# Kernel tuning notes

Measured on AMD Instinct MI355X. Metric: run time of the kernel, lower is better.

The kernel has to match this reference:

```python
import jax, jax.numpy as jnp
import numpy as np

B, L, H, HEADS, N_NODE = 1024, 200, 128, 8, 200000
MAXN = L + 1  # max_n_node
D = H // HEADS
EPS = 1e-12


def setup_inputs() -> dict:
    key = jax.random.key(0)
    ks = jax.random.split(key, 20)
    lengths = jax.random.randint(ks[0], (B,), 1, L + 1)
    mask = (jnp.arange(L)[None, :] < lengths[:, None]).astype(jnp.int32)  # contiguous 1s
    alias_inputs = jax.random.randint(ks[1], (B, L), 0, MAXN)
    items = jax.random.randint(ks[2], (B, MAXN), 0, N_NODE)

    def lin_w(k, o, i):
        return (jax.random.normal(k, (o, i), jnp.float32) * 0.1)

    inp = dict(
        alias_inputs=alias_inputs,
        items=items,
        mask=mask,
        emb_W=jax.random.normal(ks[3], (N_NODE, H), jnp.float32) * 0.1,
        # LastAttenion params
        W0=lin_w(ks[4], H, H), b0=jax.random.normal(ks[5], (H,), jnp.float32) * 0.1,
        W1=lin_w(ks[6], H, H), b1=jax.random.normal(ks[7], (H,), jnp.float32) * 0.1,
        W2=lin_w(ks[8], H, H), b2=jax.random.normal(ks[9], (H,), jnp.float32) * 0.1,
        # linear_q[0] (last_k = 1)
        Wq=lin_w(ks[10], H, H), bq=jax.random.normal(ks[11], (H,), jnp.float32) * 0.1,
        # linear_transform (2H -> H)
        Wt=lin_w(ks[12], H, 2 * H), bt=jax.random.normal(ks[13], (H,), jnp.float32) * 0.1,
        ln_g=jax.random.normal(ks[14], (H,), jnp.float32) * 0.1,
        ln_b=jax.random.normal(ks[15], (H,), jnp.float32) * 0.1,
    )
    return inp


def reference(alias_inputs, items, mask, emb_W, W0, b0, W1, b1, W2, b2, Wq, bq, Wt, bt, ln_g, ln_b):
    maskf = mask.astype(jnp.float32)
    # hidden = normalize(embedding(items)); dropout off (eval)
    hidden = emb_W[items]                                                  # [B, MAXN, H]
    hidden = hidden / (jnp.linalg.norm(hidden, axis=-1, keepdims=True) + EPS)
    # per-batch gather: seq_hidden[b, t] = hidden[b, alias_inputs[b, t]]
    seq = jnp.take_along_axis(hidden, alias_inputs[..., None], axis=1)     # [B, L, H]
    seq = seq * maskf[..., None]
    seq = seq / (jnp.linalg.norm(seq, axis=-1, keepdims=True) + EPS)
    # compute_scores
    lengths = mask.sum(1)
    last_idx = lengths - 1                                                 # >= 0 (lengths >= 1)
    ht_last = seq[jnp.arange(B), last_idx]                                 # [B, H]  (ht0 too)
    hts = (ht_last @ Wq.T + bq)[:, None, :]                                # [B, 1, H]
    # torch.norm over dim=1 (size 1) == elementwise abs
    hts = hts / (jnp.linalg.norm(hts, axis=1, keepdims=True) + EPS)
    # LastAttenion (last_k = 1, no lp-pool, eval dropout off)
    q0 = (hts @ W0.T + b0).reshape(B * HEADS, 1, D)                        # [B*h, 1, d]
    q1 = (seq @ W1.T + b1).reshape(B * HEADS, L, D)                        # [B*h, L, d]
    q2 = (seq @ W2.T + b2).reshape(B, L, HEADS, D)                         # [B, L, h, d]
    alpha = jax.nn.sigmoid(jnp.einsum('bkd,bld->bkl', q0, q1))             # [B*h, 1, L]
    alpha = alpha.reshape(B, HEADS, L).transpose(0, 2, 1)                  # [B, L, h]
    alpha = jax.nn.softmax(2.0 * alpha, axis=1)
    a = jnp.sum((alpha[..., None] * q2).reshape(B, L, H) * maskf[..., None], axis=1)  # [B, H]
    # layernorm eps=1e-8
    mu = a.mean(-1, keepdims=True)
    var = ((a - mu) ** 2).mean(-1, keepdims=True)
    a = (a - mu) / jnp.sqrt(var + 1e-8) * ln_g + ln_b
    a = jnp.concatenate([a, ht_last], axis=1) @ Wt.T + bt                  # [B, H]
    # norm=True branch
    a = a / (jnp.linalg.norm(a, axis=1, keepdims=True) + EPS)
    b = emb_W[1:]
    b = b / (jnp.linalg.norm(b, axis=1, keepdims=True) + EPS)
    return a, b.T                                                          # [B,H], [H, N_NODE-1]
```

## Files before the change

### kernel.cpp

```cpp
#include <hip/hip_runtime.h>
#include <math.h>

typedef unsigned int uint;
typedef unsigned short ushort;

__device__ __forceinline__ float b2f(ushort u){
  union { uint i; float f; } v; v.i = ((uint)u) << 16; return v.f;
}
__device__ __forceinline__ ushort f2b(float f){
  union { float f; uint i; } v; v.f = f;
  uint i = v.i;
  i += 0x7fffu + ((i >> 16) & 1u);
  return (ushort)(i >> 16);
}
__device__ __forceinline__ float wred(float v){
  #pragma unroll
  for (int s = 32; s > 0; s >>= 1) v += __shfl_xor(v, s, 64);
  return v;
}
__device__ __forceinline__ float gred16(float v){
  v += __shfl_xor(v, 1, 64);
  v += __shfl_xor(v, 2, 64);
  v += __shfl_xor(v, 4, 64);
  v += __shfl_xor(v, 8, 64);
  return v;
}
__device__ __forceinline__ float sane(float v){ return isfinite(v) ? v : 0.f; }
__device__ __forceinline__ int iclamp(int v, int lo, int hi){ return v < lo ? lo : (v > hi ? hi : v); }
__device__ __forceinline__ void cp8(float d[8], const float s[8]){
  #pragma unroll
  for (int e = 0; e < 8; ++e) d[e] = s[e];
}

__device__ __forceinline__ void load_raw8(const void* emb, int isf, int it, int p, float x[8]){
  if (it >= 0){
    if (isf){
      const float4* q = (const float4*)((const float*)emb + (size_t)it * 128);
      float4 u = q[p * 2], u2 = q[p * 2 + 1];
      x[0] = u.x; x[1] = u.y; x[2] = u.z; x[3] = u.w;
      x[4] = u2.x; x[5] = u2.y; x[6] = u2.z; x[7] = u2.w;
    } else {
      uint4 u = ((const uint4*)((const ushort*)emb + (size_t)it * 128))[p];
      x[0] = b2f((ushort)u.x); x[1] = b2f((ushort)(u.x >> 16));
      x[2] = b2f((ushort)u.y); x[3] = b2f((ushort)(u.y >> 16));
      x[4] = b2f((ushort)u.z); x[5] = b2f((ushort)(u.z >> 16));
      x[6] = b2f((ushort)u.w); x[7] = b2f((ushort)(u.w >> 16));
    }
  } else {
    #pragma unroll
    for (int e = 0; e < 8; ++e) x[e] = 0.f;
  }
}

__device__ __forceinline__ int detect_isf(const void* emb, int t, int* s_flag){
  if (t == 0) *s_flag = 0;
  __syncthreads();
  if (t < 64){
    uint4 u = ((const uint4*)emb)[t];
    uint w[4] = { u.x, u.y, u.z, u.w };
    int bad = 0;
    #pragma unroll
    for (int e = 0; e < 4; ++e){
      float v0 = fabsf(b2f((ushort)w[e]));
      float v1 = fabsf(b2f((ushort)(w[e] >> 16)));
      if (!(v0 <= 1e4f) || !(v1 <= 1e4f)) bad = 1;
    }
    if (bad) *s_flag = 1;
  }
  __syncthreads();
  return *s_flag;
}

#define OUTB 131072

#define C_W0T 0
#define C_W1  16384
#define C_W2T 32768
#define C_WQT 49152
#define C_WTT 65536
#define C_B0  98304
#define C_B1  98432
#define C_B2  98560
#define C_BQ  98688
#define C_BT  98816
#define C_G   98944
#define C_BB  99072
#define C_TOT 99200

#define KFUSED_SMEM 22784

#define NB_MAIN 1024
#define NB_BOUT 3125
#define NB_TOT  4149

__global__ __launch_bounds__(256) void k_wts(
    const void* __restrict__ emb,
    const void* W0, const void* b0, const void* W1, const void* b1,
    const void* W2, const void* b2, const void* Wq, const void* bq,
    const void* Wt, const void* bt, const void* g, const void* bb,
    float* __restrict__ wts){
  __shared__ int s_flag;
  const int t = threadIdx.x;
  const int isf = detect_isf(emb, t, &s_flag);
  int j = blockIdx.x * 256 + t;
  if (j >= C_TOT) return;
  const void* src; int si;
  if (j < 16384)      { int k = j >> 7, h = j & 127; src = W0; si = h * 128 + k; }
  else if (j < 32768) { src = W1; si = j - 16384; }
  else if (j < 49152) { int i = j - 32768; int k = i >> 7, h = i & 127; src = W2; si = h * 128 + k; }
  else if (j < 65536) { int i = j - 49152; int k = i >> 7, h = i & 127; src = Wq; si = h * 128 + k; }
  else if (j < 98304) { int i = j - 65536; int k = i >> 7, h = i & 127; src = Wt; si = h * 256 + k; }
  else {
    int i = j - 98304; int arr = i >> 7;
    const void* tab[7] = { b0, b1, b2, bq, bt, g, bb };
    src = tab[arr]; si = i & 127;
  }
  wts[j] = isf ? ((const float*)src)[si] : b2f(((const ushort*)src)[si]);
}

__device__ void bout_block(const void* __restrict__ emb, int isf,
                           void* __restrict__ outv, int bb, int t, char* dsm){
  float* tile = (float*)dsm;
  const int gid = t >> 4, p = t & 15;
  const int base = bb * 64;
  for (int pass = 0; pass < 2; ++pass){
    const int pb = base + pass * 32;
    if (pass) __syncthreads();
    for (int i = gid; i < 32; i += 16){
      int gi = pb + i;
      if (gi < 199999){
        float x[8];
        load_raw8(emb, isf, gi + 1, p, x);
        float ss = 0.f;
        #pragma unroll
        for (int e = 0; e < 8; ++e) ss += x[e] * x[e];
        ss = gred16(ss);
        float inv = 1.f / (sqrtf(ss) + 1e-12f);
        #pragma unroll
        for (int e = 0; e < 8; ++e) tile[i * 129 + p * 8 + e] = x[e] * inv;
      }
    }
    __syncthreads();
    #pragma unroll
    for (int it = 0; it < 16; ++it){
      int idx = it * 256 + t;
      int h = idx >> 5, n = idx & 31;
      int gi = pb + n;
      if (gi < 199999){
        float val = sane(tile[n * 129 + h]);
        if (isf){
          float* op = (float*)outv + OUTB + (size_t)h * 199999 + gi;
          __builtin_nontemporal_store(val, op);
        } else {
          ushort* op = (ushort*)outv + OUTB + (size_t)h * 199999 + gi;
          __builtin_nontemporal_store(f2b(val), op);
        }
      }
    }
  }
}

__global__ __launch_bounds__(256) void k_fused(
    const int* __restrict__ alias_, const int* __restrict__ items,
    const int* __restrict__ mask, const void* __restrict__ emb,
    const float* __restrict__ wts, void* __restrict__ outv){
  extern __shared__ __align__(16) char dsm[];
  __shared__ int s_flag;
  __shared__ float s_X0[128], s_ht[128], s_a[128], s_hts[128];
  __shared__ float s_c1[64];
  __shared__ float s_T[8], s_Tp[64];
  __shared__ float s_red[16];
  __shared__ float s_nrm[200];
  __shared__ int   s_it[200];
  __shared__ int   s_item;

  const int t = threadIdx.x;
  const int isf = detect_isf(emb, t, &s_flag);

  const int bid = blockIdx.x;
  const int m = (bid * NB_MAIN) / NB_TOT;
  const bool is_main = ((bid + 1) * NB_MAIN) / NB_TOT > m;
  if (!is_main){
    bout_block(emb, isf, outv, bid - m, t, dsm);
    return;
  }
  const int b = m;

  ushort* s_w1p   = (ushort*)dsm;
  float*  s_part  = (float*)dsm;
  float*  s_alpha = (float*)(dsm + 16384);

  const int wv = t >> 6, gid = t >> 4, p = t & 15, lane = t & 63;
  const int mbase = b * 200;

  int mv = 0;
  if (t < 200){
    mv = mask[mbase + t];
    int a = mv ? iclamp(alias_[mbase + t], 0, 200) : 0;
    s_it[t] = mv ? iclamp(items[b * 201 + a], 0, 199999) : -1;
  }
  float lv = wred((float)mv);
  if ((t & 63) == 0) s_red[t >> 6] = lv;
  __syncthreads();

  float xc[8], xn1[8];
  load_raw8(emb, isf, s_it[gid], p, xc);
  load_raw8(emb, isf, s_it[gid + 16], p, xn1);

  const int len = iclamp((int)(s_red[0] + s_red[1] + s_red[2] + s_red[3] + 0.5f), 1, 200);
  if (t == 0){
    int a = iclamp(alias_[mbase + len - 1], 0, 200);
    s_item = iclamp(items[b * 201 + a], 0, 199999);
  }
  __syncthreads();

  float v = 0.f;
  if (t < 128)
    v = isf ? ((const float*)emb)[(size_t)s_item * 128 + t]
            : b2f(((const ushort*)emb)[(size_t)s_item * 128 + t]);
  float ss = wred(v * v);
  if ((t & 63) == 0) s_red[4 + (t >> 6)] = ss;
  __syncthreads();
  v = v / (sqrtf(s_red[4] + s_red[5]) + 1e-12f);
  float ss2 = wred(v * v);
  if ((t & 63) == 0) s_red[8 + (t >> 6)] = ss2;
  __syncthreads();
  v = v / (sqrtf(s_red[8] + s_red[9]) + 1e-12f);
  if (t < 128) s_ht[t] = v;
  __syncthreads();

  if (t < 128){
    double d0 = 0.0, d1 = 0.0, d2 = 0.0, d3 = 0.0;
    for (int k = 0; k < 128; k += 4){
      d0 += (double)wts[C_WQT + (k    ) * 128 + t] * (double)s_ht[k    ];
      d1 += (double)wts[C_WQT + (k + 1) * 128 + t] * (double)s_ht[k + 1];
      d2 += (double)wts[C_WQT + (k + 2) * 128 + t] * (double)s_ht[k + 2];
      d3 += (double)wts[C_WQT + (k + 3) * 128 + t] * (double)s_ht[k + 3];
    }
    float a = (float)((double)wts[C_BQ + t] + ((d0 + d1) + (d2 + d3)));
    s_hts[t] = a / (fabsf(a) + 1e-12f);
  }
  __syncthreads();
  if (t < 128){
    float a0 = 0.f, a1 = 0.f, a2 = 0.f, a3 = 0.f;
    for (int k = 0; k < 128; k += 4){
      a0 += wts[C_W0T + (k    ) * 128 + t] * s_hts[k    ];
      a1 += wts[C_W0T + (k + 1) * 128 + t] * s_hts[k + 1];
      a2 += wts[C_W0T + (k + 2) * 128 + t] * s_hts[k + 2];
      a3 += wts[C_W0T + (k + 3) * 128 + t] * s_hts[k + 3];
    }
    s_X0[t] = wts[C_B0 + t] + ((a0 + a1) + (a2 + a3));
  }
  __syncthreads();
  if (t < 64){
    int head = t >> 3, j = t & 7;
    float c = 0.f;
    #pragma unroll
    for (int d = 0; d < 16; ++d) c += s_X0[head * 16 + d] * wts[C_B1 + j * 16 + d];
    s_c1[t] = c;
  }

  __syncthreads();
  for (int idx = t; idx < 8192; idx += 256){
    int hj = idx >> 7, k = idx & 127, head = hj >> 3, j = hj & 7;
    float acc = 0.f;
    const float* w1r = wts + C_W1 + (j * 16) * 128 + k;
    #pragma unroll
    for (int d = 0; d < 16; ++d) acc += s_X0[head * 16 + d] * w1r[d * 128];
    s_w1p[hj * 128 + k] = f2b(acc);
  }
  __syncthreads();

  {
    float xt[8];
    for (int r = gid; r < 200; r += 16){
      int rn = r + 32;
      load_raw8(emb, isf, rn < 200 ? s_it[rn] : -1, p, xt);

      int head = r / 25, lb = (r % 25) * 8;
      uint4 wu[8];
      #pragma unroll
      for (int j = 0; j < 8; ++j)
        wu[j] = *(const uint4*)(s_w1p + (head * 8 + j) * 128 + p * 8);

      float ssr = 0.f;
      #pragma unroll
      for (int e = 0; e < 8; ++e) ssr += xc[e] * xc[e];
      ssr = gred16(ssr);
      float inv = 1.f / (sqrtf(ssr) + 1e-12f);
      #pragma unroll
      for (int e = 0; e < 8; ++e) xc[e] *= inv;
      if (p == 0) s_nrm[r] = inv;

      #pragma unroll
      for (int j = 0; j < 8; ++j){
        float dot = xc[0] * b2f((ushort)wu[j].x) + xc[1] * b2f((ushort)(wu[j].x >> 16))
                  + xc[2] * b2f((ushort)wu[j].y) + xc[3] * b2f((ushort)(wu[j].y >> 16))
                  + xc[4] * b2f((ushort)wu[j].z) + xc[5] * b2f((ushort)(wu[j].z >> 16))
                  + xc[6] * b2f((ushort)wu[j].w) + xc[7] * b2f((ushort)(wu[j].w >> 16));
        dot = gred16(dot);
        if (p == 0){
          float logit = s_c1[head * 8 + j] + dot;
          s_alpha[(lb + j) * 8 + head] = 2.f / (1.f + expf(-logit));
        }
      }
      cp8(xc, xn1); cp8(xn1, xt);
    }
  }
  __syncthreads();

  {
    int head = t >> 5, l32 = t & 31;
    float vals[7]; float mx = -1e30f;
    #pragma unroll
    for (int i = 0; i < 7; ++i){
      int l = l32 + 32 * i;
      float xx = (l < 200) ? s_alpha[l * 8 + head] : -1e30f;
      vals[i] = xx; mx = fmaxf(mx, xx);
    }
    #pragma unroll
    for (int s = 16; s > 0; s >>= 1) mx = fmaxf(mx, __shfl_xor(mx, s, 64));
    float sum = 0.f; float e[7];
    #pragma unroll
    for (int i = 0; i < 7; ++i){
      int l = l32 + 32 * i;
      float ex = (l < 200) ? expf(vals[i] - mx) : 0.f;
      e[i] = ex; sum += ex;
    }
    #pragma unroll
    for (int s = 16; s > 0; s >>= 1) sum += __shfl_xor(sum, s, 64);
    float inv = 1.f / sum;
    #pragma unroll
    for (int i = 0; i < 7; ++i){
      int l = l32 + 32 * i;
      if (l < 200) s_alpha[l * 8 + head] = e[i] * inv;
    }
  }
  __syncthreads();

  if (t < 64){
    int h = t & 7, seg = t >> 3;
    int l0 = seg * 25, l1 = l0 + 25; if (l1 > len) l1 = len;
    float s = 0.f;
    for (int l = l0; l < l1; ++l) s += s_alpha[l * 8 + h];
    s_Tp[t] = s;
  }
  __syncthreads();
  if (t < 8){
    float s = 0.f;
    #pragma unroll
    for (int seg = 0; seg < 8; ++seg) s += s_Tp[seg * 8 + t];
    s_T[t] = s;
  }

  float acc[64];
  #pragma unroll
  for (int e = 0; e < 64; ++e) acc[e] = 0.f;
  {
    float ha[8], hb[8], ht8[8];
    load_raw8(emb, isf, s_it[gid], p, ha);
    load_raw8(emb, isf, gid + 16 < 200 ? s_it[gid + 16] : -1, p, hb);
    for (int l = gid; l < 200; l += 16){
      int lc = l + 32;
      load_raw8(emb, isf, lc < 200 ? s_it[lc] : -1, p, ht8);
      if (s_it[l] >= 0){
        float nm = s_nrm[l];
        float x[8];
        #pragma unroll
        for (int e = 0; e < 8; ++e) x[e] = ha[e] * nm;
        float4 a0 = *(const float4*)(s_alpha + l * 8);
        float4 a1 = *(const float4*)(s_alpha + l * 8 + 4);
        float al[8] = { a0.x, a0.y, a0.z, a0.w, a1.x, a1.y, a1.z, a1.w };
        #pragma unroll
        for (int h = 0; h < 8; ++h)
          #pragma unroll
          for (int e = 0; e < 8; ++e) acc[h * 8 + e] += al[h] * x[e];
      }
      cp8(ha, hb); cp8(hb, ht8);
    }
  }
  #pragma unroll
  for (int e = 0; e < 64; ++e){
    float vv = acc[e];
    vv += __shfl_xor(vv, 16, 64);
    vv += __shfl_xor(vv, 32, 64);
    acc[e] = vv;
  }
  __syncthreads();
  if (lane < 16){
    #pragma unroll
    for (int h = 0; h < 8; ++h)
      #pragma unroll
      for (int e = 0; e < 8; ++e)
        s_part[wv * 1024 + h * 128 + p * 8 + e] = acc[h * 8 + e];
  }
  __syncthreads();
  for (int i = t; i < 1024; i += 256)
    s_part[i] = s_part[i] + s_part[1024 + i] + s_part[2048 + i] + s_part[3072 + i];
  __syncthreads();

  float araw = 0.f;
  if (t < 128){
    int head = t >> 4;
    const float* hl = &s_part[head * 128];
    float a0 = 0.f, a1 = 0.f, a2 = 0.f, a3 = 0.f;
    for (int k = 0; k < 128; k += 4){
      a0 += hl[k    ] * wts[C_W2T + (k    ) * 128 + t];
      a1 += hl[k + 1] * wts[C_W2T + (k + 1) * 128 + t];
      a2 += hl[k + 2] * wts[C_W2T + (k + 2) * 128 + t];
      a3 += hl[k + 3] * wts[C_W2T + (k + 3) * 128 + t];
    }
    araw = wts[C_B2 + t] * s_T[head] + ((a0 + a1) + (a2 + a3));
  }
  float v1 = wred(t < 128 ? araw : 0.f);
  if ((t & 63) == 0) s_red[t >> 6] = v1;
  __syncthreads();
  float mu = (s_red[0] + s_red[1]) * 0.0078125f;
  float dd = (t < 128) ? (araw - mu) : 0.f;
  float v2 = wred(dd * dd);
  if ((t & 63) == 0) s_red[4 + (t >> 6)] = v2;
  __syncthreads();
  float var = (s_red[4] + s_red[5]) * 0.0078125f;
  if (t < 128)
    s_a[t] = dd / sqrtf(var + 1e-8f) * wts[C_G + t] + wts[C_BB + t];
  __syncthreads();

  float o = 0.f;
  if (t < 128){
    float o0 = 0.f, o1 = 0.f, o2 = 0.f, o3 = 0.f;
    for (int k = 0; k < 128; k += 2){
      o0 += s_a[k    ] * wts[C_WTT + (k      ) * 128 + t];
      o1 += s_a[k + 1] * wts[C_WTT + (k + 1  ) * 128 + t];
      o2 += s_ht[k   ] * wts[C_WTT + (128 + k) * 128 + t];
      o3 += s_ht[k+ 1] * wts[C_WTT + (129 + k) * 128 + t];
    }
    o = wts[C_BT + t] + ((o0 + o1) + (o2 + o3));
  }
  float v3 = wred(t < 128 ? o * o : 0.f);
  if ((t & 63) == 0) s_red[8 + (t >> 6)] = v3;
  __syncthreads();
  float nrm = sqrtf(s_red[8] + s_red[9]);
  if (t < 128){
    float val = sane(o / (nrm + 1e-12f));
    if (isf) ((float*)outv)[b * 128 + t] = val;
    else     ((ushort*)outv)[b * 128 + t] = f2b(val);
  }
}

extern "C" void kernel_launch(void* const* d_in, const int* in_sizes, int n_in,
                              void* d_out, int out_size, void* d_ws, size_t ws_size,
                              hipStream_t stream){
  const int* alias_ = (const int*)d_in[0];
  const int* items  = (const int*)d_in[1];
  const int* mask   = (const int*)d_in[2];
  const void* emb = d_in[3];
  const void* W0  = d_in[4];
  const void* b0  = d_in[5];
  const void* W1  = d_in[6];
  const void* b1  = d_in[7];
  const void* W2  = d_in[8];
  const void* b2_ = d_in[9];
  const void* Wq  = d_in[10];
  const void* bq  = d_in[11];
  const void* Wt  = d_in[12];
  const void* bt  = d_in[13];
  const void* g_  = d_in[14];
  const void* bb_ = d_in[15];

  char* ws = (char*)d_ws;
  float* wts = (float*)ws;

  static int g_attr_done = 0;
  if (!g_attr_done){
    hipError_t e = hipFuncSetAttribute(reinterpret_cast<const void*>(k_fused),
                        hipFuncAttributeMaxDynamicSharedMemorySize, KFUSED_SMEM);
    (void)e;
    g_attr_done = 1;
  }

  k_wts  <<<dim3(388),    dim3(256), 0,           stream>>>(emb, W0, b0, W1, b1,
                                                  W2, b2_, Wq, bq, Wt, bt, g_, bb_, wts);
  k_fused<<<dim3(NB_TOT), dim3(256), KFUSED_SMEM, stream>>>(alias_, items, mask, emb,
                                                  wts, d_out);
}
```

Baseline: 362.0 us.

## Pack two batch rows per 512-thread block and widen output-transpose blocks

Moves the fused kernel to 512-thread blocks. Each main block now handles two batch rows in independent 256-thread halves with separate shared-memory slots, which halves the main block count. The b-output transpose blocks use the extra threads to do each 32-row pass in one step. This is meant to cut per-block overhead and improve latency hiding, at the cost of doubled LDS per block. The 64-float per-thread accumulator under a 512 launch bound may also cause register pressure or spills.

Result: slower. 635.6 us (+75.6%).

```diff
diff --git a/kernel.cpp b/kernel.cpp
--- a/kernel.cpp
+++ b/kernel.cpp
@@ -87,11 +87,12 @@
 #define C_BB  99072
 #define C_TOT 99200
 
-#define KFUSED_SMEM 22784
-
-#define NB_MAIN 1024
-#define NB_BOUT 3125
-#define NB_TOT  4149
+#define SLOT_SZ 22784
+#define KFUSED_SMEM (2 * SLOT_SZ)
+
+#define NB_MAINB 512
+#define NB_BOUT  3125
+#define NB_TOT   (NB_MAINB + NB_BOUT)
 
 __global__ __launch_bounds__(256) void k_wts(
     const void* __restrict__ emb,
@@ -126,8 +127,8 @@
   for (int pass = 0; pass < 2; ++pass){
     const int pb = base + pass * 32;
     if (pass) __syncthreads();
-    for (int i = gid; i < 32; i += 16){
-      int gi = pb + i;
+    {
+      int gi = pb + gid;
       if (gi < 199999){
         float x[8];
         load_raw8(emb, isf, gi + 1, p, x);
@@ -137,13 +138,13 @@
         ss = gred16(ss);
         float inv = 1.f / (sqrtf(ss) + 1e-12f);
         #pragma unroll
-        for (int e = 0; e < 8; ++e) tile[i * 129 + p * 8 + e] = x[e] * inv;
+        for (int e = 0; e < 8; ++e) tile[gid * 129 + p * 8 + e] = x[e] * inv;
       }
     }
     __syncthreads();
     #pragma unroll
-    for (int it = 0; it < 16; ++it){
-      int idx = it * 256 + t;
+    for (int it = 0; it < 8; ++it){
+      int idx = it * 512 + t;
       int h = idx >> 5, n = idx & 31;
       int gi = pb + n;
       if (gi < 199999){
@@ -160,113 +161,118 @@
   }
 }
 
-__global__ __launch_bounds__(256) void k_fused(
+__global__ __launch_bounds__(512) void k_fused(
     const int* __restrict__ alias_, const int* __restrict__ items,
     const int* __restrict__ mask, const void* __restrict__ emb,
     const float* __restrict__ wts, void* __restrict__ outv){
   extern __shared__ __align__(16) char dsm[];
   __shared__ int s_flag;
-  __shared__ float s_X0[128], s_ht[128], s_a[128], s_hts[128];
-  __shared__ float s_c1[64];
-  __shared__ float s_T[8], s_Tp[64];
-  __shared__ float s_red[16];
-  __shared__ float s_nrm[200];
-  __shared__ int   s_it[200];
-  __shared__ int   s_item;
+  __shared__ float s_X0[2][128], s_ht[2][128], s_a[2][128], s_hts[2][128];
+  __shared__ float s_c1[2][64];
+  __shared__ float s_T[2][8], s_Tp[2][64];
+  __shared__ float s_red[2][16];
+  __shared__ float s_nrm[2][200];
+  __shared__ int   s_it[2][200];
+  __shared__ int   s_item[2];
 
   const int t = threadIdx.x;
   const int isf = detect_isf(emb, t, &s_flag);
 
   const int bid = blockIdx.x;
-  const int m = (bid * NB_MAIN) / NB_TOT;
-  const bool is_main = ((bid + 1) * NB_MAIN) / NB_TOT > m;
+  const int m = (bid * NB_MAINB) / NB_TOT;
+  const bool is_main = ((bid + 1) * NB_MAINB) / NB_TOT > m;
   if (!is_main){
     bout_block(emb, isf, outv, bid - m, t, dsm);
     return;
   }
-  const int b = m;
-
-  ushort* s_w1p   = (ushort*)dsm;
-  float*  s_part  = (float*)dsm;
-  float*  s_alpha = (float*)(dsm + 16384);
-
-  const int wv = t >> 6, gid = t >> 4, p = t & 15, lane = t & 63;
+
+  const int half = t >> 8;
+  const int tb = t & 255;
+  const int b = m * 2 + half;
+
+  char* mydsm = dsm + half * SLOT_SZ;
+  ushort* s_w1p   = (ushort*)mydsm;
+  float*  s_part  = (float*)mydsm;
+  float*  s_alpha = (float*)(mydsm + 16384);
+
+  const int wv = tb >> 6, gid = tb >> 4, p = tb & 15, lane = tb & 63;
   const int mbase = b * 200;
 
   int mv = 0;
-  if (t < 200){
-    mv = mask[mbase + t];
-    int a = mv ? iclamp(alias_[mbase + t], 0, 200) : 0;
-    s_it[t] = mv ? iclamp(items[b * 201 + a], 0, 199999) : -1;
+  if (tb < 200){
+    mv = mask[mbase + tb];
+    int a = mv ? iclamp(alias_[mbase + tb], 0, 200) : 0;
+    s_it[half][tb] = mv ? iclamp(items[b * 201 + a], 0, 199999) : -1;
   }
   float lv = wred((float)mv);
-  if ((t & 63) == 0) s_red[t >> 6] = lv;
+  if ((tb & 63) == 0) s_red[half][tb >> 6] = lv;
   __syncthreads();
 
   float xc[8], xn1[8];
-  load_raw8(emb, isf, s_it[gid], p, xc);
-  load_raw8(emb, isf, s_it[gid + 16], p, xn1);
-
-  const int len = iclamp((int)(s_red[0] + s_red[1] + s_red[2] + s_red[3] + 0.5f), 1, 200);
-  if (t == 0){
+  load_raw8(emb, isf, s_it[half][gid], p, xc);
+  load_raw8(emb, isf, s_it[half][gid + 16], p, xn1);
+
+  const int len = iclamp((int)(s_red[half][0] + s_red[half][1] +
+                               s_red[half][2] + s_red[half][3] + 0.5f), 1, 200);
+  if (tb == 0){
     int a = iclamp(alias_[mbase + len - 1], 0, 200);
-    s_item = iclamp(items[b * 201 + a], 0, 199999);
+    s_item[half] = iclamp(items[b * 201 + a], 0, 199999);
   }
   __syncthreads();
 
   float v = 0.f;
-  if (t < 128)
-    v = isf ? ((const float*)emb)[(size_t)s_item * 128 + t]
-            : b2f(((const ushort*)emb)[(size_t)s_item * 128 + t]);
+  if (tb < 128)
+    v = isf ? ((const float*)emb)[(size_t)s_item[half] * 128 + tb]
+            : b2f(((const ushort*)emb)[(size_t)s_item[half] * 128 + tb]);
   float ss = wred(v * v);
-  if ((t & 63) == 0) s_red[4 + (t >> 6)] = ss;
-  __syncthreads();
-  v = v / (sqrtf(s_red[4] + s_red[5]) + 1e-12f);
+  if ((tb & 63) == 0) s_red[half][4 + (tb >> 6)] = ss;
+  __syncthreads();
+  v = v / (sqrtf(s_red[half][4] + s_red[half][5]) + 1e-12f);
   float ss2 = wred(v * v);
-  if ((t & 63) == 0) s_red[8 + (t >> 6)] = ss2;
-  __syncthreads();
-  v = v / (sqrtf(s_red[8] + s_red[9]) + 1e-12f);
-  if (t < 128) s_ht[t] = v;
-  __syncthreads();
-
-  if (t < 128){
+  if ((tb & 63) == 0) s_red[half][8 + (tb >> 6)] = ss2;
+  __syncthreads();
+  v = v / (sqrtf(s_red[half][8] + s_red[half][9]) + 1e-12f);
+  if (tb < 128) s_ht[half][tb] = v;
+  __syncthreads();
+
+  if (tb < 128){
     double d0 = 0.0, d1 = 0.0, d2 = 0.0, d3 = 0.0;
     for (int k = 0; k < 128; k += 4){
-      d0 += (double)wts[C_WQT + (k    ) * 128 + t] * (double)s_ht[k    ];
-      d1 += (double)wts[C_WQT + (k + 1) * 128 + t] * (double)s_ht[k + 1];
-      d2 += (double)wts[C_WQT + (k + 2) * 128 + t] * (double)s_ht[k + 2];
-      d3 += (double)wts[C_WQT + (k + 3) * 128 + t] * (double)s_ht[k + 3];
-    }
-    float a = (float)((double)wts[C_BQ + t] + ((d0 + d1) + (d2 + d3)));
-    s_hts[t] = a / (fabsf(a) + 1e-12f);
-  }
-  __syncthreads();
-  if (t < 128){
+      d0 += (double)wts[C_WQT + (k    ) * 128 + tb] * (double)s_ht[half][k    ];
+      d1 += (double)wts[C_WQT + (k + 1) * 128 + tb] * (double)s_ht[half][k + 1];
+      d2 += (double)wts[C_WQT + (k + 2) * 128 + tb] * (double)s_ht[half][k + 2];
+      d3 += (double)wts[C_WQT + (k + 3) * 128 + tb] * (double)s_ht[half][k + 3];
+    }
+    float a = (float)((double)wts[C_BQ + tb] + ((d0 + d1) + (d2 + d3)));
+    s_hts[half][tb] = a / (fabsf(a) + 1e-12f);
+  }
+  __syncthreads();
+  if (tb < 128){
     float a0 = 0.f, a1 = 0.f, a2 = 0.f, a3 = 0.f;
     for (int k = 0; k < 128; k += 4){
-      a0 += wts[C_W0T + (k    ) * 128 + t] * s_hts[k    ];
-      a1 += wts[C_W0T + (k + 1) * 128 + t] * s_hts[k + 1];
-      a2 += wts[C_W0T + (k + 2) * 128 + t] * s_hts[k + 2];
-      a3 += wts[C_W0T + (k + 3) * 128 + t] * s_hts[k + 3];
-    }
-    s_X0[t] = wts[C_B0 + t] + ((a0 + a1) + (a2 + a3));
-  }
-  __syncthreads();
-  if (t < 64){
-    int head = t >> 3, j = t & 7;
+      a0 += wts[C_W0T + (k    ) * 128 + tb] * s_hts[half][k    ];
+      a1 += wts[C_W0T + (k + 1) * 128 + tb] * s_hts[half][k + 1];
+      a2 += wts[C_W0T + (k + 2) * 128 + tb] * s_hts[half][k + 2];
+      a3 += wts[C_W0T + (k + 3) * 128 + tb] * s_hts[half][k + 3];
+    }
+    s_X0[half][tb] = wts[C_B0 + tb] + ((a0 + a1) + (a2 + a3));
+  }
+  __syncthreads();
+  if (tb < 64){
+    int head = tb >> 3, j = tb & 7;
     float c = 0.f;
     #pragma unroll
-    for (int d = 0; d < 16; ++d) c += s_X0[head * 16 + d] * wts[C_B1 + j * 16 + d];
-    s_c1[t] = c;
-  }
-
-  __syncthreads();
-  for (int idx = t; idx < 8192; idx += 256){
+    for (int d = 0; d < 16; ++d) c += s_X0[half][head * 16 + d] * wts[C_B1 + j * 16 + d];
+    s_c1[half][tb] = c;
+  }
+
+  __syncthreads();
+  for (int idx = tb; idx < 8192; idx += 256){
     int hj = idx >> 7, k = idx & 127, head = hj >> 3, j = hj & 7;
     float acc = 0.f;
     const float* w1r = wts + C_W1 + (j * 16) * 128 + k;
     #pragma unroll
-    for (int d = 0; d < 16; ++d) acc += s_X0[head * 16 + d] * w1r[d * 128];
+    for (int d = 0; d < 16; ++d) acc += s_X0[half][head * 16 + d] * w1r[d * 128];
     s_w1p[hj * 128 + k] = f2b(acc);
   }
   __syncthreads();
@@ -275,7 +281,7 @@
     float xt[8];
     for (int r = gid; r < 200; r += 16){
       int rn = r + 32;
-      load_raw8(emb, isf, rn < 200 ? s_it[rn] : -1, p, xt);
+      load_raw8(emb, isf, rn < 200 ? s_it[half][rn] : -1, p, xt);
 
       int head = r / 25, lb = (r % 25) * 8;
       uint4 wu[8];
@@ -290,7 +296,7 @@
       float inv = 1.f / (sqrtf(ssr) + 1e-12f);
       #pragma unroll
       for (int e = 0; e < 8; ++e) xc[e] *= inv;
-      if (p == 0) s_nrm[r] = inv;
+      if (p == 0) s_nrm[half][r] = inv;
 
       #pragma unroll
       for (int j = 0; j < 8; ++j){
@@ -300,7 +306,7 @@
                   + xc[6] * b2f((ushort)wu[j].w) + xc[7] * b2f((ushort)(wu[j].w >> 16));
         dot = gred16(dot);
         if (p == 0){
-          float logit = s_c1[head * 8 + j] + dot;
+          float logit = s_c1[half][head * 8 + j] + dot;
           s_alpha[(lb + j) * 8 + head] = 2.f / (1.f + expf(-logit));
         }
       }
@@ -310,7 +316,7 @@
   __syncthreads();
 
   {
-    int head = t >> 5, l32 = t & 31;
+    int head = tb >> 5, l32 = tb & 31;
     float vals[7]; float mx = -1e30f;
     #pragma unroll
     for (int i = 0; i < 7; ++i){
@@ -338,19 +344,19 @@
   }
   __syncthreads();
 
-  if (t < 64){
-    int h = t & 7, seg = t >> 3;
+  if (tb < 64){
+    int h = tb & 7, seg = tb >> 3;
     int l0 = seg * 25, l1 = l0 + 25; if (l1 > len) l1 = len;
     float s = 0.f;
     for (int l = l0; l < l1; ++l) s += s_alpha[l * 8 + h];
-    s_Tp[t] = s;
-  }
-  __syncthreads();
-  if (t < 8){
+    s_Tp[half][tb] = s;
+  }
+  __syncthreads();
+  if (tb < 8){
     float s = 0.f;
     #pragma unroll
-    for (int seg = 0; seg < 8; ++seg) s += s_Tp[seg * 8 + t];
-    s_T[t] = s;
+    for (int seg = 0; seg < 8; ++seg) s += s_Tp[half][seg * 8 + tb];
+    s_T[half][tb] = s;
   }
 
   float acc[64];
@@ -358,13 +364,13 @@
   for (int e = 0; e < 64; ++e) acc[e] = 0.f;
   {
     float ha[8], hb[8], ht8[8];
-    load_raw8(emb, isf, s_it[gid], p, ha);
-    load_raw8(emb, isf, gid + 16 < 200 ? s_it[gid + 16] : -1, p, hb);
+    load_raw8(emb, isf, s_it[half][gid], p, ha);
+    load_raw8(emb, isf, gid + 16 < 200 ? s_it[half][gid + 16] : -1, p, hb);
     for (int l = gid; l < 200; l += 16){
       int lc = l + 32;
-      load_raw8(emb, isf, lc < 200 ? s_it[lc] : -1, p, ht8);
-      if (s_it[l] >= 0){
-        float nm = s_nrm[l];
+      load_raw8(emb, isf, lc < 200 ? s_it[half][lc] : -1, p, ht8);
+      if (s_it[half][l] >= 0){
+        float nm = s_nrm[half][l];
         float x[8];
         #pragma unroll
         for (int e = 0; e < 8; ++e) x[e] = ha[e] * nm;
@@ -395,55 +401,55 @@
         s_part[wv * 1024 + h * 128 + p * 8 + e] = acc[h * 8 + e];
   }
   __syncthreads();
-  for (int i = t; i < 1024; i += 256)
+  for (int i = tb; i < 1024; i += 256)
     s_part[i] = s_part[i] + s_part[1024 + i] + s_part[2048 + i] + s_part[3072 + i];
   __syncthreads();
 
   float araw = 0.f;
-  if (t < 128){
-    int head = t >> 4;
+  if (tb < 128){
+    int head = tb >> 4;
     const float* hl = &s_part[head * 128];
     float a0 = 0.f, a1 = 0.f, a2 = 0.f, a3 = 0.f;
     for (int k = 0; k < 128; k += 4){
-      a0 += hl[k    ] * wts[C_W2T + (k    ) * 128 + t];
-      a1 += hl[k + 1] * wts[C_W2T + (k + 1) * 128 + t];
-      a2 += hl[k + 2] * wts[C_W2T + (k + 2) * 128 + t];
-      a3 += hl[k + 3] * wts[C_W2T + (k + 3) * 128 + t];
-    }
-    araw = wts[C_B2 + t] * s_T[head] + ((a0 + a1) + (a2 + a3));
-  }
-  float v1 = wred(t < 128 ? araw : 0.f);
-  if ((t & 63) == 0) s_red[t >> 6] = v1;
-  __syncthreads();
-  float mu = (s_red[0] + s_red[1]) * 0.0078125f;
-  float dd = (t < 128) ? (araw - mu) : 0.f;
+      a0 += hl[k    ] * wts[C_W2T + (k    ) * 128 + tb];
+      a1 += hl[k + 1] * wts[C_W2T + (k + 1) * 128 + tb];
+      a2 += hl[k + 2] * wts[C_W2T + (k + 2) * 128 + tb];
+      a3 += hl[k + 3] * wts[C_W2T + (k + 3) * 128 + tb];
+    }
+    araw = wts[C_B2 + tb] * s_T[half][head] + ((a0 + a1) + (a2 + a3));
+  }
+  float v1 = wred(tb < 128 ? araw : 0.f);
+  if ((tb & 63) == 0) s_red[half][tb >> 6] = v1;
+  __syncthreads();
+  float mu = (s_red[half][0] + s_red[half][1]) * 0.0078125f;
+  float dd = (tb < 128) ? (araw - mu) : 0.f;
   float v2 = wred(dd * dd);
-  if ((t & 63) == 0) s_red[4 + (t >> 6)] = v2;
-  __syncthreads();
-  float var = (s_red[4] + s_red[5]) * 0.0078125f;
-  if (t < 128)
-    s_a[t] = dd / sqrtf(var + 1e-8f) * wts[C_G + t] + wts[C_BB + t];
+  if ((tb & 63) == 0) s_red[half][4 + (tb >> 6)] = v2;
+  __syncthreads();
+  float var = (s_red[half][4] + s_red[half][5]) * 0.0078125f;
+  if (tb < 128)
+    s_a[half][tb] = dd / sqrtf(var + 1e-8f) * wts[C_G + tb] + wts[C_BB + tb];
   __syncthreads();
 
   float o = 0.f;
-  if (t < 128){
+  if (tb < 128){
     float o0 = 0.f, o1 = 0.f, o2 = 0.f, o3 = 0.f;
     for (int k = 0; k < 128; k += 2){
-      o0 += s_a[k    ] * wts[C_WTT + (k      ) * 128 + t];
-      o1 += s_a[k + 1] * wts[C_WTT + (k + 1  ) * 128 + t];
-      o2 += s_ht[k   ] * wts[C_WTT + (128 + k) * 128 + t];
-      o3 += s_ht[k+ 1] * wts[C_WTT + (129 + k) * 128 + t];
-    }
-    o = wts[C_BT + t] + ((o0 + o1) + (o2 + o3));
-  }
-  float v3 = wred(t < 128 ? o * o : 0.f);
-  if ((t & 63) == 0) s_red[8 + (t >> 6)] = v3;
-  __syncthreads();
-  float nrm = sqrtf(s_red[8] + s_red[9]);
-  if (t < 128){
+      o0 += s_a[half][k    ] * wts[C_WTT + (k      ) * 128 + tb];
+      o1 += s_a[half][k + 1] * wts[C_WTT + (k + 1  ) * 128 + tb];
+      o2 += s_ht[half][k   ] * wts[C_WTT + (128 + k) * 128 + tb];
+      o3 += s_ht[half][k+ 1] * wts[C_WTT + (129 + k) * 128 + tb];
+    }
+    o = wts[C_BT + tb] + ((o0 + o1) + (o2 + o3));
+  }
+  float v3 = wred(tb < 128 ? o * o : 0.f);
+  if ((tb & 63) == 0) s_red[half][8 + (tb >> 6)] = v3;
+  __syncthreads();
+  float nrm = sqrtf(s_red[half][8] + s_red[half][9]);
+  if (tb < 128){
     float val = sane(o / (nrm + 1e-12f));
-    if (isf) ((float*)outv)[b * 128 + t] = val;
-    else     ((ushort*)outv)[b * 128 + t] = f2b(val);
+    if (isf) ((float*)outv)[b * 128 + tb] = val;
+    else     ((ushort*)outv)[b * 128 + tb] = f2b(val);
   }
 }
 
@@ -480,6 +486,6 @@
 
   k_wts  <<<dim3(388),    dim3(256), 0,           stream>>>(emb, W0, b0, W1, b1,
                                                   W2, b2_, Wq, bq, Wt, bt, g_, bb_, wts);
-  k_fused<<<dim3(NB_TOT), dim3(256), KFUSED_SMEM, stream>>>(alias_, items, mask, emb,
+  k_fused<<<dim3(NB_TOT), dim3(512), KFUSED_SMEM, stream>>>(alias_, items, mask, emb,
                                                   wts, d_out);
 }
```
